# Optimization experiments

Hardware: AMD Instinct MI355X
Metric: run time of the kernel (lower is better)

## Reference

```python
import jax, jax.numpy as jnp
import numpy as np

N_NODES = 100000
F_IN = 512
HIDDEN = 64
N_CLASS = 40
N_EDGES = 3200000


def gcn_conv(x, src, dst, deg_inv_sqrt, W, b, n_nodes):
    # PyG GCNConv: linear transform, then deg^{-1/2} A_hat deg^{-1/2} aggregation, then bias
    h = x @ W  # [N, out]
    norm = deg_inv_sqrt[src] * deg_inv_sqrt[dst]  # [E+N] (includes self-loops)
    msg = h[src] * norm[:, None]  # gather + scale
    out = jax.ops.segment_sum(msg, dst, num_segments=n_nodes)  # scatter-add
    return out + b


def setup_inputs() -> dict:
    key = jax.random.key(0)
    k1, k2, k3, k4, k5 = jax.random.split(key, 5)
    x = jax.random.normal(k1, (N_NODES, F_IN), dtype=jnp.float32)
    edge_index = jax.random.randint(k2, (2, N_EDGES), 0, N_NODES, dtype=jnp.int64)
    # Glorot-style init for GCN weights
    W1 = jax.random.normal(k3, (F_IN, HIDDEN), dtype=jnp.float32) / np.sqrt(F_IN)
    b1 = jnp.zeros((HIDDEN,), dtype=jnp.float32)
    W2 = jax.random.normal(k4, (HIDDEN, N_CLASS), dtype=jnp.float32) / np.sqrt(HIDDEN)
    b2 = jnp.zeros((N_CLASS,), dtype=jnp.float32)
    return {"x": x, "edge_index": edge_index, "W1": W1, "b1": b1, "W2": W2, "b2": b2}


def reference(x, edge_index, W1, b1, W2, b2):
    n = x.shape[0]
    loops = jnp.arange(n, dtype=edge_index.dtype)
    src = jnp.concatenate([edge_index[0], loops])  # add self-loops (GCNConv default)
    dst = jnp.concatenate([edge_index[1], loops])
    deg = jax.ops.segment_sum(jnp.ones_like(dst, dtype=x.dtype), dst, num_segments=n)
    deg_inv_sqrt = jnp.where(deg > 0, jax.lax.rsqrt(deg), 0.0)
    h = gcn_conv(x, src, dst, deg_inv_sqrt, W1, b1, n)
    h = jax.nn.relu(h)  # dropout treated as eval-mode identity
    x_out = gcn_conv(h, src, dst, deg_inv_sqrt, W2, b2, n)
    return jax.nn.log_softmax(x_out, axis=1), x_out
```

## Files before the change

### kernel.cpp

```cpp
#include <hip/hip_runtime.h>
#include <math.h>

#define N_NODES 100000
#define F_IN    512
#define HIDDEN  64
#define N_CLASS 40
#define N_EDGES 3200000
#define NB      782
#define CAP     6144
#define EPB     8192
#define NPB     391

typedef int EIdx;

typedef __attribute__((ext_vector_type(8))) short short8;
typedef __attribute__((ext_vector_type(4))) float f32x4;
typedef __attribute__((ext_vector_type(4))) unsigned uint4v;

__device__ inline short f2bf(float f) {
    unsigned u = __builtin_bit_cast(unsigned, f);
    unsigned r = u + 0x7FFFu + ((u >> 16) & 1u);
    return (short)(r >> 16);
}

__device__ inline unsigned cvtpk(float lo, float hi) {
    unsigned r;
    asm("v_cvt_pk_bf16_f32 %0, %1, %2" : "=v"(r) : "v"(lo), "v"(hi));
    return r;
}

__device__ inline float bflo(unsigned w) { return __builtin_bit_cast(float, w << 16); }
__device__ inline float bfhi(unsigned w) { return __builtin_bit_cast(float, w & 0xFFFF0000u); }

__global__ __launch_bounds__(256) void binit_kernel(int* __restrict__ bcur) {
    int i = blockIdx.x * 256 + threadIdx.x;
    if (i < NB) bcur[i] = i * CAP;
}

__global__ __launch_bounds__(256) void part1_kernel(const EIdx* __restrict__ src,
                                                    const EIdx* __restrict__ dst,
                                                    int* __restrict__ bcur,
                                                    unsigned* __restrict__ bpacked) {
    __shared__ int hist[NB];
    __shared__ int excl[NB];
    __shared__ int cur[NB];
    __shared__ int delta[NB];
    __shared__ int stmp[256];
    __shared__ unsigned spk[EPB];
    __shared__ unsigned short bid[EPB];
    int t = threadIdx.x;
    int e0 = blockIdx.x * EPB;
    for (int j = t; j < NB; j += 256) hist[j] = 0;
    __syncthreads();
#pragma unroll 4
    for (int k = 0; k < 32; ++k) {
        int e = e0 + k * 256 + t;
        if (e < N_EDGES) atomicAdd(&hist[dst[e] >> 7], 1);
    }
    __syncthreads();
    {
        int i0 = 4 * t;
        int v0 = (i0 < NB) ? hist[i0] : 0;
        int v1 = (i0 + 1 < NB) ? hist[i0 + 1] : 0;
        int v2 = (i0 + 2 < NB) ? hist[i0 + 2] : 0;
        int v3 = (i0 + 3 < NB) ? hist[i0 + 3] : 0;
        int s = v0 + v1 + v2 + v3;
        stmp[t] = s;
        __syncthreads();
        for (int o = 1; o < 256; o <<= 1) {
            int a = (t >= o) ? stmp[t - o] : 0;
            __syncthreads();
            stmp[t] += a;
            __syncthreads();
        }
        int E = stmp[t] - s;
        if (i0 < NB) excl[i0] = E;
        if (i0 + 1 < NB) excl[i0 + 1] = E + v0;
        if (i0 + 2 < NB) excl[i0 + 2] = E + v0 + v1;
        if (i0 + 3 < NB) excl[i0 + 3] = E + v0 + v1 + v2;
    }
    __syncthreads();
    for (int j = t; j < NB; j += 256) {
        int h = hist[j];
        int rsv = h ? atomicAdd(&bcur[j], h) : 0;
        delta[j] = rsv - excl[j];
        cur[j] = excl[j];
    }
    __syncthreads();
#pragma unroll 4
    for (int k = 0; k < 32; ++k) {
        int e = e0 + k * 256 + t;
        if (e < N_EDGES) {
            int d = dst[e], s = src[e];
            int b = d >> 7;
            int p = atomicAdd(&cur[b], 1);
            spk[p] = ((unsigned)(d & 127) << 20) | (unsigned)s;
            bid[p] = (unsigned short)b;
        }
    }
    __syncthreads();
    int cnt = N_EDGES - e0;
    if (cnt > EPB) cnt = EPB;
    for (int i = t; i < cnt; i += 256) {
        int bb = bid[i];
        int pos = i + delta[bb];
        if (pos < (bb + 1) * CAP) bpacked[pos] = spk[i];
    }
}

__global__ __launch_bounds__(256) void part2_kernel(const int* __restrict__ bcur,
                                                    const unsigned* __restrict__ bpacked,
                                                    int* __restrict__ csr_src,
                                                    unsigned* __restrict__ rowmeta,
                                                    float* __restrict__ dis) {
    __shared__ unsigned ent[CAP];
    __shared__ int hist[128];
    __shared__ int stmp[128];
    __shared__ int cur[128];
    int t = threadIdx.x;
    int bk = blockIdx.x;
    int base = bk * CAP;
    int cnt = bcur[bk] - base;
    if (cnt > CAP) cnt = CAP;
    if (t < 128) hist[t] = 0;
    __syncthreads();
    for (int i = t; i < cnt; i += 256) {
        unsigned p = bpacked[base + i];
        ent[i] = p;
        atomicAdd(&hist[p >> 20], 1);
    }
    __syncthreads();
    if (t < 128) stmp[t] = hist[t];
    __syncthreads();
    for (int o = 1; o < 128; o <<= 1) {
        int a = (t >= o && t < 128) ? stmp[t - o] : 0;
        __syncthreads();
        if (t < 128) stmp[t] += a;
        __syncthreads();
    }
    if (t < 128) {
        int ex = stmp[t] - hist[t];
        cur[t] = ex;
        int n = (bk << 7) + t;
        if (n < N_NODES) {
            rowmeta[n] = (unsigned)(base + ex) | ((unsigned)hist[t] << 23);
            dis[n] = rsqrtf((float)(hist[t] + 1));
        }
    }
    __syncthreads();
    for (int i = t; i < cnt; i += 256) {
        unsigned p = ent[i];
        int p2 = atomicAdd(&cur[p >> 20], 1);
        csr_src[base + p2] = (int)(p & 0xFFFFFu);
    }
}

__global__ __launch_bounds__(256) void wprep_kernel(const float* __restrict__ W,
                                                    short* __restrict__ Wbf) {
    int idx = blockIdx.x * 256 + threadIdx.x;
    int k = idx >> 6, col = idx & 63;
    Wbf[col * F_IN + (k ^ ((col & 7) << 3))] = f2bf(W[idx]);
}

__global__ __launch_bounds__(256) void gemm1_mfma_kernel(const float* __restrict__ x,
                                                         const short* __restrict__ Wbf,
                                                         const float* __restrict__ dis,
                                                         unsigned* __restrict__ h1b) {
    __shared__ short Wt[HIDDEN * 256];
    int tid = threadIdx.x;
    int wave = tid >> 6, lane = tid & 63;
    int r0 = blockIdx.x * 128 + wave * 32;
    int lrow = lane & 15;
    int lk = (lane >> 4) * 8;
    int bswz = (lane & 7) << 3;

    f32x4 acc[2][4];
#pragma unroll
    for (int m = 0; m < 2; ++m)
#pragma unroll
        for (int n = 0; n < 4; ++n) acc[m][n] = (f32x4)0.0f;

    int rowA0 = r0 + lrow;       if (rowA0 >= N_NODES) rowA0 = N_NODES - 1;
    int rowA1 = r0 + 16 + lrow;  if (rowA1 >= N_NODES) rowA1 = N_NODES - 1;
    const float* pA0 = x + (size_t)rowA0 * F_IN + lk;
    const float* pA1 = x + (size_t)rowA1 * F_IN + lk;

    const short8* Wv = (const short8*)Wbf;
    short8* Lv = (short8*)Wt;

    for (int kh = 0; kh < 2; ++kh) {
        __syncthreads();
        for (int i = tid; i < 2048; i += 256)
            Lv[i] = Wv[(i >> 5) * 64 + kh * 32 + (i & 31)];
        __syncthreads();
        for (int k0 = 0; k0 < 256; k0 += 32) {
            int kg = kh * 256 + k0;
            short8 a0, a1;
            {
                float4 v0 = *reinterpret_cast<const float4*>(pA0 + kg);
                float4 v1 = *reinterpret_cast<const float4*>(pA0 + kg + 4);
                uint4v u = {cvtpk(v0.x, v0.y), cvtpk(v0.z, v0.w),
                            cvtpk(v1.x, v1.y), cvtpk(v1.z, v1.w)};
                a0 = __builtin_bit_cast(short8, u);
            }
            {
                float4 v0 = *reinterpret_cast<const float4*>(pA1 + kg);
                float4 v1 = *reinterpret_cast<const float4*>(pA1 + kg + 4);
                uint4v u = {cvtpk(v0.x, v0.y), cvtpk(v0.z, v0.w),
                            cvtpk(v1.x, v1.y), cvtpk(v1.z, v1.w)};
                a1 = __builtin_bit_cast(short8, u);
            }
            short8 b[4];
#pragma unroll
            for (int n = 0; n < 4; ++n) {
                int c = n * 16 + lrow;
                int si = c * 256 + ((k0 + lk) ^ bswz);
                b[n] = *reinterpret_cast<const short8*>(&Wt[si]);
            }
#pragma unroll
            for (int n = 0; n < 4; ++n) {
                acc[0][n] = __builtin_amdgcn_mfma_f32_16x16x32_bf16(a0, b[n], acc[0][n], 0, 0, 0);
                acc[1][n] = __builtin_amdgcn_mfma_f32_16x16x32_bf16(a1, b[n], acc[1][n], 0, 0, 0);
            }
        }
    }

    int crow = (lane >> 4) * 4, ccol = lane & 15;
    bool evenc = (ccol & 1) == 0;
#pragma unroll
    for (int m = 0; m < 2; ++m) {
#pragma unroll
        for (int j = 0; j < 4; ++j) {
            int rr = r0 + m * 16 + crow + j;
            int rs = (rr < N_NODES) ? rr : (N_NODES - 1);
            float ds = dis[rs];
            float v[4], vn[4];
#pragma unroll
            for (int n = 0; n < 4; ++n) v[n] = acc[m][n][j] * ds;
#pragma unroll
            for (int n = 0; n < 4; ++n) vn[n] = __shfl_xor(v[n], 1);
            if (rr < N_NODES && evenc) {
#pragma unroll
                for (int n = 0; n < 4; ++n)
                    h1b[(size_t)rr * 32 + ((n * 16 + ccol) >> 1)] = cvtpk(v[n], vn[n]);
            }
        }
    }
}

__global__ __launch_bounds__(256) void gather1_kernel(const unsigned* __restrict__ h1b,
                                                      const unsigned* __restrict__ rowmeta,
                                                      const int* __restrict__ csr_src,
                                                      const float* __restrict__ dis,
                                                      const float* __restrict__ b,
                                                      float* __restrict__ out) {
    int n = blockIdx.x * 4 + (threadIdx.x >> 6);
    int lane = threadIdx.x & 63;
    int g = lane >> 4, l = lane & 15;
    unsigned meta = rowmeta[n];
    int i = (int)(meta & 0x7FFFFFu);
    int i1 = i + (int)(meta >> 23);
    float ax = 0.f, ay = 0.f, az = 0.f, aw = 0.f;
    if (g == 0) {
        uint2 v = *reinterpret_cast<const uint2*>(h1b + (size_t)n * 32 + 2 * l);
        ax = bflo(v.x); ay = bfhi(v.x); az = bflo(v.y); aw = bfhi(v.y);
    }
    for (; i + 15 < i1; i += 16) {
        int s0 = csr_src[i + g], s1 = csr_src[i + 4 + g];
        int s2 = csr_src[i + 8 + g], s3 = csr_src[i + 12 + g];
        uint2 r0 = *reinterpret_cast<const uint2*>(h1b + (size_t)s0 * 32 + 2 * l);
        uint2 r1 = *reinterpret_cast<const uint2*>(h1b + (size_t)s1 * 32 + 2 * l);
        uint2 r2 = *reinterpret_cast<const uint2*>(h1b + (size_t)s2 * 32 + 2 * l);
        uint2 r3 = *reinterpret_cast<const uint2*>(h1b + (size_t)s3 * 32 + 2 * l);
        ax += (bflo(r0.x) + bflo(r1.x)) + (bflo(r2.x) + bflo(r3.x));
        ay += (bfhi(r0.x) + bfhi(r1.x)) + (bfhi(r2.x) + bfhi(r3.x));
        az += (bflo(r0.y) + bflo(r1.y)) + (bflo(r2.y) + bflo(r3.y));
        aw += (bfhi(r0.y) + bfhi(r1.y)) + (bfhi(r2.y) + bfhi(r3.y));
    }
    for (; i < i1; i += 4) {
        if (i + g < i1) {
            int s = csr_src[i + g];
            uint2 r = *reinterpret_cast<const uint2*>(h1b + (size_t)s * 32 + 2 * l);
            ax += bflo(r.x); ay += bfhi(r.x); az += bflo(r.y); aw += bfhi(r.y);
        }
    }
    ax += __shfl_xor(ax, 16); ax += __shfl_xor(ax, 32);
    ay += __shfl_xor(ay, 16); ay += __shfl_xor(ay, 32);
    az += __shfl_xor(az, 16); az += __shfl_xor(az, 32);
    aw += __shfl_xor(aw, 16); aw += __shfl_xor(aw, 32);
    if (lane < 16) {
        float ds = dis[n];
        float4 bb = *reinterpret_cast<const float4*>(b + 4 * l);
        float4 o = {fmaxf(fmaf(ax, ds, bb.x), 0.f), fmaxf(fmaf(ay, ds, bb.y), 0.f),
                    fmaxf(fmaf(az, ds, bb.z), 0.f), fmaxf(fmaf(aw, ds, bb.w), 0.f)};
        *reinterpret_cast<float4*>(out + (size_t)n * HIDDEN + 4 * l) = o;
    }
}

__global__ __launch_bounds__(256) void gemm2_kernel(const float* __restrict__ x,
                                                    const float* __restrict__ W,
                                                    const float* __restrict__ dis,
                                                    unsigned* __restrict__ h2b) {
    int r = blockIdx.x * 256 + threadIdx.x;
    if (r >= N_NODES) return;
    float acc[N_CLASS];
#pragma unroll
    for (int j = 0; j < N_CLASS; ++j) acc[j] = 0.0f;
    const float* xr = x + (size_t)r * HIDDEN;
    for (int k0 = 0; k0 < HIDDEN; k0 += 4) {
        float4 xv = *reinterpret_cast<const float4*>(xr + k0);
        const float* wk = W + (size_t)k0 * N_CLASS;
#pragma unroll
        for (int j = 0; j < N_CLASS; ++j) {
            acc[j] = fmaf(xv.x, wk[j], acc[j]);
            acc[j] = fmaf(xv.y, wk[N_CLASS + j], acc[j]);
            acc[j] = fmaf(xv.z, wk[2 * N_CLASS + j], acc[j]);
            acc[j] = fmaf(xv.w, wk[3 * N_CLASS + j], acc[j]);
        }
    }
    float ds = dis[r];
    unsigned* hr = h2b + (size_t)r * 20;
#pragma unroll
    for (int q = 0; q < 5; ++q) {
        uint4v o = {cvtpk(acc[8 * q] * ds,     acc[8 * q + 1] * ds),
                    cvtpk(acc[8 * q + 2] * ds, acc[8 * q + 3] * ds),
                    cvtpk(acc[8 * q + 4] * ds, acc[8 * q + 5] * ds),
                    cvtpk(acc[8 * q + 6] * ds, acc[8 * q + 7] * ds)};
        *reinterpret_cast<uint4v*>(hr + 4 * q) = o;
    }
}

__global__ __launch_bounds__(256) void gather2_kernel(const unsigned* __restrict__ h2b,
                                                      const unsigned* __restrict__ rowmeta,
                                                      const int* __restrict__ csr_src,
                                                      const float* __restrict__ dis,
                                                      const float* __restrict__ b,
                                                      float* __restrict__ xout,
                                                      float* __restrict__ out_ls) {
    int n = blockIdx.x * 4 + (threadIdx.x >> 6);
    int lane = threadIdx.x & 63;
    int g = lane >> 4, l = lane & 15;
    bool al = l < 10;
    unsigned meta = rowmeta[n];
    int i = (int)(meta & 0x7FFFFFu);
    int i1 = i + (int)(meta >> 23);
    float ax = 0.f, ay = 0.f, az = 0.f, aw = 0.f;
    if (g == 0 && al) {
        uint2 v = *reinterpret_cast<const uint2*>(h2b + (size_t)n * 20 + 2 * l);
        ax = bflo(v.x); ay = bfhi(v.x); az = bflo(v.y); aw = bfhi(v.y);
    }
    for (; i + 15 < i1; i += 16) {
        int s0 = csr_src[i + g], s1 = csr_src[i + 4 + g];
        int s2 = csr_src[i + 8 + g], s3 = csr_src[i + 12 + g];
        if (al) {
            uint2 r0 = *reinterpret_cast<const uint2*>(h2b + (size_t)s0 * 20 + 2 * l);
            uint2 r1 = *reinterpret_cast<const uint2*>(h2b + (size_t)s1 * 20 + 2 * l);
            uint2 r2 = *reinterpret_cast<const uint2*>(h2b + (size_t)s2 * 20 + 2 * l);
            uint2 r3 = *reinterpret_cast<const uint2*>(h2b + (size_t)s3 * 20 + 2 * l);
            ax += (bflo(r0.x) + bflo(r1.x)) + (bflo(r2.x) + bflo(r3.x));
            ay += (bfhi(r0.x) + bfhi(r1.x)) + (bfhi(r2.x) + bfhi(r3.x));
            az += (bflo(r0.y) + bflo(r1.y)) + (bflo(r2.y) + bflo(r3.y));
            aw += (bfhi(r0.y) + bfhi(r1.y)) + (bfhi(r2.y) + bfhi(r3.y));
        }
    }
    for (; i < i1; i += 4) {
        if (al && i + g < i1) {
            int s = csr_src[i + g];
            uint2 r = *reinterpret_cast<const uint2*>(h2b + (size_t)s * 20 + 2 * l);
            ax += bflo(r.x); ay += bfhi(r.x); az += bflo(r.y); aw += bfhi(r.y);
        }
    }
    ax += __shfl_xor(ax, 16); ax += __shfl_xor(ax, 32);
    ay += __shfl_xor(ay, 16); ay += __shfl_xor(ay, 32);
    az += __shfl_xor(az, 16); az += __shfl_xor(az, 32);
    aw += __shfl_xor(aw, 16); aw += __shfl_xor(aw, 32);

    float ds = dis[n];
    float vx = 0.f, vy = 0.f, vz = 0.f, vw = 0.f;
    if (al) {
        float4 bb = *reinterpret_cast<const float4*>(b + 4 * l);
        vx = fmaf(ax, ds, bb.x); vy = fmaf(ay, ds, bb.y);
        vz = fmaf(az, ds, bb.z); vw = fmaf(aw, ds, bb.w);
    }
    float mx = al ? fmaxf(fmaxf(vx, vy), fmaxf(vz, vw)) : -INFINITY;
#pragma unroll
    for (int o = 8; o > 0; o >>= 1) mx = fmaxf(mx, __shfl_xor(mx, o));
    float e = al ? (expf(vx - mx) + expf(vy - mx)) + (expf(vz - mx) + expf(vw - mx)) : 0.0f;
    float sum = e;
#pragma unroll
    for (int o = 8; o > 0; o >>= 1) sum += __shfl_xor(sum, o);
    if (g == 0 && al) {
        float ls = mx + logf(sum);
        float4 xo = {vx, vy, vz, vw};
        float4 lo = {vx - ls, vy - ls, vz - ls, vw - ls};
        *reinterpret_cast<float4*>(xout + (size_t)n * N_CLASS + 4 * l) = xo;
        *reinterpret_cast<float4*>(out_ls + (size_t)n * N_CLASS + 4 * l) = lo;
    }
}

extern "C" void kernel_launch(void* const* d_in, const int* in_sizes, int n_in,
                              void* d_out, int out_size, void* d_ws, size_t ws_size,
                              hipStream_t stream) {
    const float* x  = (const float*)d_in[0];
    const EIdx*  ei = (const EIdx*)d_in[1];
    const float* W1 = (const float*)d_in[2];
    const float* b1 = (const float*)d_in[3];
    const float* W2 = (const float*)d_in[4];
    const float* b2 = (const float*)d_in[5];
    const EIdx* src = ei;
    const EIdx* dst = ei + N_EDGES;

    float* out_ls = (float*)d_out;
    float* x_out  = out_ls + (size_t)N_NODES * N_CLASS;

    char* w = (char*)d_ws;
    int*      bcur    = (int*)w;       w += 1024 * 4;
    float*    dis     = (float*)w;     w += 100352 * 4;
    unsigned* rowmeta = (unsigned*)w;  w += 100352 * 4;
    short*    Wbf     = (short*)w;     w += (size_t)F_IN * HIDDEN * 2;
    unsigned* bpacked = (unsigned*)w;
    float*    agg1    = (float*)w;     w += (size_t)N_NODES * HIDDEN * 4;
    int*      csr_src = (int*)w;       w += (size_t)NB * CAP * 4;
    unsigned* h1b     = (unsigned*)w;  w += (size_t)N_NODES * 32 * 4;
    unsigned* h2b     = (unsigned*)w;  w += (size_t)N_NODES * 20 * 4;

    const int B = 256;
    int gN  = (N_NODES + B - 1) / B;
    int gW  = N_NODES / 4;
    int gM1 = (N_NODES + 127) / 128;

    binit_kernel<<<4, B, 0, stream>>>(bcur);
    part1_kernel<<<NPB, B, 0, stream>>>(src, dst, bcur, bpacked);
    part2_kernel<<<NB, B, 0, stream>>>(bcur, bpacked, csr_src, rowmeta, dis);
    wprep_kernel<<<(F_IN * HIDDEN) / B, B, 0, stream>>>(W1, Wbf);

    gemm1_mfma_kernel<<<gM1, B, 0, stream>>>(x, Wbf, dis, h1b);
    gather1_kernel<<<gW, B, 0, stream>>>(h1b, rowmeta, csr_src, dis, b1, agg1);

    gemm2_kernel<<<gN, B, 0, stream>>>(agg1, W2, dis, h2b);
    gather2_kernel<<<gW, B, 0, stream>>>(h2b, rowmeta, csr_src, dis, b2, x_out, out_ls);
}
```

Baseline: 286.1 us.

## Fuse gather1 with gemm2, stage x tiles through LDS in gemm1, cache dst in part1

The layer-1 aggregation kernel now also applies bias, ReLU and the 64x40 W2 projection per node from shared memory, so the agg1 intermediate and the separate gemm2 launch go away. gemm1 now loads x with coalesced row-chunk loads into an LDS bf16 tile, prefetching the next k-slice into registers and staging W in 128-wide k chunks. part1 keeps dst values in registers between the histogram and scatter passes so dst is not read twice. The costs are more syncthreads in gemm1, W2 reloaded into LDS by every gather block, and higher register use in part1.

New measurement: 303.0 us. +5.9%, slower.

```diff
diff --git a/kernel.cpp b/kernel.cpp
--- a/kernel.cpp
+++ b/kernel.cpp
@@ -50,12 +50,14 @@
     __shared__ unsigned short bid[EPB];
     int t = threadIdx.x;
     int e0 = blockIdx.x * EPB;
+    int dreg[32];
     for (int j = t; j < NB; j += 256) hist[j] = 0;
     __syncthreads();
-#pragma unroll 4
+#pragma unroll
     for (int k = 0; k < 32; ++k) {
         int e = e0 + k * 256 + t;
-        if (e < N_EDGES) atomicAdd(&hist[dst[e] >> 7], 1);
+        dreg[k] = (e < N_EDGES) ? dst[e] : -1;
+        if (dreg[k] >= 0) atomicAdd(&hist[dreg[k] >> 7], 1);
     }
     __syncthreads();
     {
@@ -87,11 +89,12 @@
         cur[j] = excl[j];
     }
     __syncthreads();
-#pragma unroll 4
+#pragma unroll
     for (int k = 0; k < 32; ++k) {
-        int e = e0 + k * 256 + t;
-        if (e < N_EDGES) {
-            int d = dst[e], s = src[e];
+        int d = dreg[k];
+        if (d >= 0) {
+            int e = e0 + k * 256 + t;
+            int s = src[e];
             int b = d >> 7;
             int p = atomicAdd(&cur[b], 1);
             spk[p] = ((unsigned)(d & 127) << 20) | (unsigned)s;
@@ -166,10 +169,12 @@
                                                          const short* __restrict__ Wbf,
                                                          const float* __restrict__ dis,
                                                          unsigned* __restrict__ h1b) {
-    __shared__ short Wt[HIDDEN * 256];
+    __shared__ short Wt[HIDDEN * 128];
+    __shared__ short xs[128 * 40];
     int tid = threadIdx.x;
     int wave = tid >> 6, lane = tid & 63;
-    int r0 = blockIdx.x * 128 + wave * 32;
+    int r0 = blockIdx.x * 128;
+    int wr0 = r0 + wave * 32;
     int lrow = lane & 15;
     int lk = (lane >> 4) * 8;
     int bswz = (lane & 7) << 3;
@@ -180,48 +185,62 @@
 #pragma unroll
         for (int n = 0; n < 4; ++n) acc[m][n] = (f32x4)0.0f;
 
-    int rowA0 = r0 + lrow;       if (rowA0 >= N_NODES) rowA0 = N_NODES - 1;
-    int rowA1 = r0 + 16 + lrow;  if (rowA1 >= N_NODES) rowA1 = N_NODES - 1;
-    const float* pA0 = x + (size_t)rowA0 * F_IN + lk;
-    const float* pA1 = x + (size_t)rowA1 * F_IN + lk;
+    int srow = 0, schunk = 0;
+    {
+        int idx0 = tid;
+        srow = idx0 >> 3;
+        schunk = idx0 & 7;
+    }
+    int grow[4];
+#pragma unroll
+    for (int i = 0; i < 4; ++i) {
+        int r = r0 + srow + i * 32;
+        grow[i] = (r < N_NODES) ? r : (N_NODES - 1);
+    }
+
+    float4 xr[4];
+#pragma unroll
+    for (int i = 0; i < 4; ++i)
+        xr[i] = *reinterpret_cast<const float4*>(x + (size_t)grow[i] * F_IN + 4 * schunk);
 
     const short8* Wv = (const short8*)Wbf;
     short8* Lv = (short8*)Wt;
 
-    for (int kh = 0; kh < 2; ++kh) {
+    for (int ks = 0; ks < 16; ++ks) {
+        int kg = ks * 32;
         __syncthreads();
-        for (int i = tid; i < 2048; i += 256)
-            Lv[i] = Wv[(i >> 5) * 64 + kh * 32 + (i & 31)];
+#pragma unroll
+        for (int i = 0; i < 4; ++i) {
+            uint2 u = {cvtpk(xr[i].x, xr[i].y), cvtpk(xr[i].z, xr[i].w)};
+            *reinterpret_cast<uint2*>(&xs[(srow + i * 32) * 40 + 4 * schunk]) = u;
+        }
+        if ((kg & 127) == 0) {
+            int q = kg >> 7;
+            for (int i = tid; i < 1024; i += 256) {
+                int col = i >> 4, kc = i & 15;
+                Lv[i] = Wv[col * 64 + q * 16 + kc];
+            }
+        }
         __syncthreads();
-        for (int k0 = 0; k0 < 256; k0 += 32) {
-            int kg = kh * 256 + k0;
-            short8 a0, a1;
-            {
-                float4 v0 = *reinterpret_cast<const float4*>(pA0 + kg);
-                float4 v1 = *reinterpret_cast<const float4*>(pA0 + kg + 4);
-                uint4v u = {cvtpk(v0.x, v0.y), cvtpk(v0.z, v0.w),
-                            cvtpk(v1.x, v1.y), cvtpk(v1.z, v1.w)};
-                a0 = __builtin_bit_cast(short8, u);
-            }
-            {
-                float4 v0 = *reinterpret_cast<const float4*>(pA1 + kg);
-                float4 v1 = *reinterpret_cast<const float4*>(pA1 + kg + 4);
-                uint4v u = {cvtpk(v0.x, v0.y), cvtpk(v0.z, v0.w),
-                            cvtpk(v1.x, v1.y), cvtpk(v1.z, v1.w)};
-                a1 = __builtin_bit_cast(short8, u);
-            }
-            short8 b[4];
-#pragma unroll
-            for (int n = 0; n < 4; ++n) {
-                int c = n * 16 + lrow;
-                int si = c * 256 + ((k0 + lk) ^ bswz);
-                b[n] = *reinterpret_cast<const short8*>(&Wt[si]);
-            }
-#pragma unroll
-            for (int n = 0; n < 4; ++n) {
-                acc[0][n] = __builtin_amdgcn_mfma_f32_16x16x32_bf16(a0, b[n], acc[0][n], 0, 0, 0);
-                acc[1][n] = __builtin_amdgcn_mfma_f32_16x16x32_bf16(a1, b[n], acc[1][n], 0, 0, 0);
-            }
+        if (ks < 15) {
+            int kn = kg + 32;
+#pragma unroll
+            for (int i = 0; i < 4; ++i)
+                xr[i] = *reinterpret_cast<const float4*>(x + (size_t)grow[i] * F_IN + kn + 4 * schunk);
+        }
+        int k0loc = kg & 127;
+        short8 a0 = *reinterpret_cast<const short8*>(&xs[(wave * 32 + lrow) * 40 + lk]);
+        short8 a1 = *reinterpret_cast<const short8*>(&xs[(wave * 32 + 16 + lrow) * 40 + lk]);
+        short8 b[4];
+#pragma unroll
+        for (int n = 0; n < 4; ++n) {
+            int c = n * 16 + lrow;
+            b[n] = *reinterpret_cast<const short8*>(&Wt[c * 128 + ((k0loc + lk) ^ bswz)]);
+        }
+#pragma unroll
+        for (int n = 0; n < 4; ++n) {
+            acc[0][n] = __builtin_amdgcn_mfma_f32_16x16x32_bf16(a0, b[n], acc[0][n], 0, 0, 0);
+            acc[1][n] = __builtin_amdgcn_mfma_f32_16x16x32_bf16(a1, b[n], acc[1][n], 0, 0, 0);
         }
     }
 
@@ -231,7 +250,7 @@
     for (int m = 0; m < 2; ++m) {
 #pragma unroll
         for (int j = 0; j < 4; ++j) {
-            int rr = r0 + m * 16 + crow + j;
+            int rr = wr0 + m * 16 + crow + j;
             int rs = (rr < N_NODES) ? rr : (N_NODES - 1);
             float ds = dis[rs];
             float v[4], vn[4];
@@ -248,14 +267,20 @@
     }
 }
 
-__global__ __launch_bounds__(256) void gather1_kernel(const unsigned* __restrict__ h1b,
-                                                      const unsigned* __restrict__ rowmeta,
-                                                      const int* __restrict__ csr_src,
-                                                      const float* __restrict__ dis,
-                                                      const float* __restrict__ b,
-                                                      float* __restrict__ out) {
-    int n = blockIdx.x * 4 + (threadIdx.x >> 6);
-    int lane = threadIdx.x & 63;
+__global__ __launch_bounds__(256) void gather1_gemm2_kernel(const unsigned* __restrict__ h1b,
+                                                            const unsigned* __restrict__ rowmeta,
+                                                            const int* __restrict__ csr_src,
+                                                            const float* __restrict__ dis,
+                                                            const float* __restrict__ b1,
+                                                            const float* __restrict__ W2,
+                                                            unsigned* __restrict__ h2b) {
+    __shared__ float W2s[HIDDEN * N_CLASS];
+    __shared__ float aggs[4 * HIDDEN];
+    int tid = threadIdx.x;
+    for (int i = tid; i < HIDDEN * N_CLASS; i += 256) W2s[i] = W2[i];
+
+    int wave = tid >> 6, lane = tid & 63;
+    int n = blockIdx.x * 4 + wave;
     int g = lane >> 4, l = lane & 15;
     unsigned meta = rowmeta[n];
     int i = (int)(meta & 0x7FFFFFu);
@@ -288,46 +313,25 @@
     ay += __shfl_xor(ay, 16); ay += __shfl_xor(ay, 32);
     az += __shfl_xor(az, 16); az += __shfl_xor(az, 32);
     aw += __shfl_xor(aw, 16); aw += __shfl_xor(aw, 32);
-    if (lane < 16) {
-        float ds = dis[n];
-        float4 bb = *reinterpret_cast<const float4*>(b + 4 * l);
+    float ds = dis[n];
+    if (g == 0) {
+        float4 bb = *reinterpret_cast<const float4*>(b1 + 4 * l);
         float4 o = {fmaxf(fmaf(ax, ds, bb.x), 0.f), fmaxf(fmaf(ay, ds, bb.y), 0.f),
                     fmaxf(fmaf(az, ds, bb.z), 0.f), fmaxf(fmaf(aw, ds, bb.w), 0.f)};
-        *reinterpret_cast<float4*>(out + (size_t)n * HIDDEN + 4 * l) = o;
-    }
-}
-
-__global__ __launch_bounds__(256) void gemm2_kernel(const float* __restrict__ x,
-                                                    const float* __restrict__ W,
-                                                    const float* __restrict__ dis,
-                                                    unsigned* __restrict__ h2b) {
-    int r = blockIdx.x * 256 + threadIdx.x;
-    if (r >= N_NODES) return;
-    float acc[N_CLASS];
-#pragma unroll
-    for (int j = 0; j < N_CLASS; ++j) acc[j] = 0.0f;
-    const float* xr = x + (size_t)r * HIDDEN;
-    for (int k0 = 0; k0 < HIDDEN; k0 += 4) {
-        float4 xv = *reinterpret_cast<const float4*>(xr + k0);
-        const float* wk = W + (size_t)k0 * N_CLASS;
-#pragma unroll
-        for (int j = 0; j < N_CLASS; ++j) {
-            acc[j] = fmaf(xv.x, wk[j], acc[j]);
-            acc[j] = fmaf(xv.y, wk[N_CLASS + j], acc[j]);
-            acc[j] = fmaf(xv.z, wk[2 * N_CLASS + j], acc[j]);
-            acc[j] = fmaf(xv.w, wk[3 * N_CLASS + j], acc[j]);
-        }
-    }
-    float ds = dis[r];
-    unsigned* hr = h2b + (size_t)r * 20;
-#pragma unroll
-    for (int q = 0; q < 5; ++q) {
-        uint4v o = {cvtpk(acc[8 * q] * ds,     acc[8 * q + 1] * ds),
-                    cvtpk(acc[8 * q + 2] * ds, acc[8 * q + 3] * ds),
-                    cvtpk(acc[8 * q + 4] * ds, acc[8 * q + 5] * ds),
-                    cvtpk(acc[8 * q + 6] * ds, acc[8 * q + 7] * ds)};
-        *reinterpret_cast<uint4v*>(hr + 4 * q) = o;
-    }
+        *reinterpret_cast<float4*>(&aggs[wave * HIDDEN + 4 * l]) = o;
+    }
+    __syncthreads();
+    int c = lane;
+    float out = 0.f;
+    if (c < N_CLASS) {
+#pragma unroll 8
+        for (int k = 0; k < HIDDEN; ++k)
+            out = fmaf(aggs[wave * HIDDEN + k], W2s[k * N_CLASS + c], out);
+        out *= ds;
+    }
+    float outn = __shfl_xor(out, 1);
+    if (c < N_CLASS && (c & 1) == 0)
+        h2b[(size_t)n * 20 + (c >> 1)] = cvtpk(out, outn);
 }
 
 __global__ __launch_bounds__(256) void gather2_kernel(const unsigned* __restrict__ h2b,
@@ -419,13 +423,11 @@
     unsigned* rowmeta = (unsigned*)w;  w += 100352 * 4;
     short*    Wbf     = (short*)w;     w += (size_t)F_IN * HIDDEN * 2;
     unsigned* bpacked = (unsigned*)w;
-    float*    agg1    = (float*)w;     w += (size_t)N_NODES * HIDDEN * 4;
+    unsigned* h1b     = (unsigned*)w;  w += (size_t)NB * CAP * 4;
     int*      csr_src = (int*)w;       w += (size_t)NB * CAP * 4;
-    unsigned* h1b     = (unsigned*)w;  w += (size_t)N_NODES * 32 * 4;
     unsigned* h2b     = (unsigned*)w;  w += (size_t)N_NODES * 20 * 4;
 
     const int B = 256;
-    int gN  = (N_NODES + B - 1) / B;
     int gW  = N_NODES / 4;
     int gM1 = (N_NODES + 127) / 128;
 
@@ -435,8 +437,7 @@
     wprep_kernel<<<(F_IN * HIDDEN) / B, B, 0, stream>>>(W1, Wbf);
 
     gemm1_mfma_kernel<<<gM1, B, 0, stream>>>(x, Wbf, dis, h1b);
-    gather1_kernel<<<gW, B, 0, stream>>>(h1b, rowmeta, csr_src, dis, b1, agg1);
-
-    gemm2_kernel<<<gN, B, 0, stream>>>(agg1, W2, dis, h2b);
+    gather1_gemm2_kernel<<<gW, B, 0, stream>>>(h1b, rowmeta, csr_src, dis, b1, W2, h2b);
+
     gather2_kernel<<<gW, B, 0, stream>>>(h2b, rowmeta, csr_src, dis, b2, x_out, out_ls);
 }
```
